# Performance work log

Measured on AMD Instinct MI355X. Metric: run time of the kernel, lower is better.

Reference implementation:

```python
import jax, jax.numpy as jnp
import numpy as np

S, L, E, H, HID, T = 4096, 16, 256, 512, 512, 50
CHAR_V = 128


def _lstm_scan(x, W_ih, W_hh, b):
    """x: [T, B, D] -> all hidden states [T, B, H]. PyTorch gate order i,f,g,o.
    b is the sum of torch's b_ih + b_hh (identical math)."""
    Hh = W_hh.shape[1]
    B = x.shape[1]

    def cell(carry, xt):
        h, c = carry
        g = xt @ W_ih.T + h @ W_hh.T + b  # [B, 4H]
        i, f, gg, o = jnp.split(g, 4, axis=-1)
        c = jax.nn.sigmoid(f) * c + jax.nn.sigmoid(i) * jnp.tanh(gg)
        h = jax.nn.sigmoid(o) * jnp.tanh(c)
        return (h, c), h

    init = (jnp.zeros((B, Hh), x.dtype), jnp.zeros((B, Hh), x.dtype))
    _, hs = jax.lax.scan(cell, init, x)
    return hs


def setup_inputs() -> dict:
    key = jax.random.key(0)
    ks = jax.random.split(key, 18)

    def p(k, shape):
        return jax.random.normal(k, shape, jnp.float32) * 0.05

    return {
        "chars": jax.random.randint(ks[0], (S, L), 0, CHAR_V),
        "char_lens": jax.random.randint(ks[1], (S,), 0, L),
        "char_table": p(ks[2], (CHAR_V, E)),
        "cW_ih": p(ks[3], (4 * E, E)),
        "cW_hh": p(ks[4], (4 * E, E)),
        "cb": p(ks[5], (4 * E,)),
        "W_ih0": p(ks[6], (2, 4 * H, E)),
        "W_hh0": p(ks[7], (2, 4 * H, H)),
        "b0": p(ks[8], (2, 4 * H)),
        "W_ih1": p(ks[9], (2, 4 * H, 2 * H)),
        "W_hh1": p(ks[10], (2, 4 * H, H)),
        "b1": p(ks[11], (2, 4 * H)),
        "fc1_w": p(ks[12], (HID, 2 * H)),
        "fc1_b": p(ks[13], (HID,)),
        "fc2_w": p(ks[14], (T, HID)),
        "fc2_b": p(ks[15], (T,)),
    }


def reference(chars, char_lens, char_table, cW_ih, cW_hh, cb,
              W_ih0, W_hh0, b0, W_ih1, W_hh1, b1,
              fc1_w, fc1_b, fc2_w, fc2_b):
    n_words = chars.shape[0]
    # --- char LSTM: batched over all words (replaces per-word python loop) ---
    emb = char_table[chars]                               # [S, L, E]
    hs = _lstm_scan(emb.transpose(1, 0, 2), cW_ih, cW_hh, cb)  # [L, S, E]
    lens = jnp.maximum(char_lens, 1)                      # every word has >=1 char
    word_emb = hs[lens - 1, jnp.arange(n_words)]          # hn per word: [S, E]

    # --- 2-layer bidirectional sentence LSTM, batch = 1 ---
    x = word_emb[:, None, :]                              # [S, 1, E]

    def bi_layer(x, Wih, Whh, b):
        fwd = _lstm_scan(x, Wih[0], Whh[0], b[0])
        bwd = _lstm_scan(x[::-1], Wih[1], Whh[1], b[1])[::-1]
        return jnp.concatenate([fwd, bwd], axis=-1)       # [S, 1, 2H]

    x = bi_layer(x, W_ih0, W_hh0, b0)
    x = bi_layer(x, W_ih1, W_hh1, b1)

    # --- MLP head ---
    out = x[:, 0, :]                                      # [S, 2H]
    out = jnp.tanh(out @ fc1_w.T + fc1_b)                 # [S, HID]
    return out @ fc2_w.T + fc2_b                          # [S, T]
```

## Files before the change

### kernel.cpp

```cpp
#include <hip/hip_runtime.h>
#include <math.h>
#include <stdint.h>


#define NPOS 4096
#define GDIM 2048

typedef short short8 __attribute__((ext_vector_type(8)));
typedef float f32x4 __attribute__((ext_vector_type(4)));

__device__ __forceinline__ float sigf(float x) { return 1.0f / (1.0f + __expf(-x)); }
__device__ __forceinline__ float tanh_fast(float x) {
  float e = __expf(2.f * x);
  return 1.f - 2.f / (e + 1.f);
}
__device__ __forceinline__ unsigned int pack_bf16(float a, float b) {
  unsigned int ua = __float_as_uint(a), ub = __float_as_uint(b);
  ua = (ua + 0x7fffu + ((ua >> 16) & 1u)) >> 16;
  ub = (ub + 0x7fffu + ((ub >> 16) & 1u)) >> 16;
  return ua | (ub << 16);
}
__device__ __forceinline__ unsigned short bf16_1(float a) {
  unsigned int ua = __float_as_uint(a);
  return (unsigned short)((ua + 0x7fffu + ((ua >> 16) & 1u)) >> 16);
}
__device__ __forceinline__ float bf2f(unsigned short s) {
  return __uint_as_float(((unsigned int)s) << 16);
}

__global__ __launch_bounds__(256) void build_wc_kernel(
    const float* __restrict__ cWih, const float* __restrict__ cWhh,
    unsigned int* __restrict__ Wc)
{
  const int idx = blockIdx.x * 256 + threadIdx.x;
  const int g = idx >> 8;
  const int k = (idx & 255) * 2;
  const float* src = (k < 256) ? (cWih + (size_t)g * 256 + k)
                               : (cWhh + (size_t)g * 256 + (k - 256));
  Wc[idx] = pack_bf16(src[0], src[1]);
}

__global__ __launch_bounds__(256) void mfchar_kernel(
    const int* __restrict__ chars, const int* __restrict__ lens,
    const float* __restrict__ table, const unsigned short* __restrict__ Wc,
    const float* __restrict__ cb, float* __restrict__ word_emb)
{
  __shared__ unsigned short uL[32][520];
  __shared__ unsigned short gL[32][1032];
  __shared__ int sidx[32];
  const int tid = threadIdx.x;
  const int lane = tid & 63;
  const int wv = tid >> 6;
  const int w0 = blockIdx.x * 32;
  if (tid < 32) { int l = lens[w0 + tid]; sidx[tid] = (l < 1 ? 1 : l) - 1; }
  for (int i = tid; i < 32 * 256; i += 256) uL[i >> 8][256 + (i & 255)] = 0;

  float bz[16];
  #pragma unroll
  for (int ni = 0; ni < 16; ++ni) bz[ni] = cb[wv * 256 + ni * 16 + (lane & 15)];

  float c[32];
  #pragma unroll
  for (int w = 0; w < 32; ++w) c[w] = 0.f;

  const int arow = lane & 15;
  const int akk = (lane >> 4) * 8;

  for (int t = 0; t < 16; ++t) {
    for (int w = 0; w < 32; ++w) {
      const int cid = chars[(w0 + w) * 16 + t];
      uL[w][tid] = bf16_1(table[(size_t)cid * 256 + tid]);
    }
    __syncthreads();

    f32x4 acc[2][16];
    #pragma unroll
    for (int mi = 0; mi < 2; ++mi)
      #pragma unroll
      for (int ni = 0; ni < 16; ++ni)
        acc[mi][ni] = (f32x4){bz[ni], bz[ni], bz[ni], bz[ni]};
    for (int kt = 0; kt < 16; ++kt) {
      short8 af0 = *(const short8*)&uL[arow][kt * 32 + akk];
      short8 af1 = *(const short8*)&uL[16 + arow][kt * 32 + akk];
      #pragma unroll
      for (int ni = 0; ni < 16; ++ni) {
        const unsigned short* bp =
            Wc + (size_t)(wv * 256 + ni * 16 + arow) * 512 + kt * 32 + akk;
        short8 bf = *(const short8*)bp;
        acc[0][ni] = __builtin_amdgcn_mfma_f32_16x16x32_bf16(af0, bf, acc[0][ni], 0, 0, 0);
        acc[1][ni] = __builtin_amdgcn_mfma_f32_16x16x32_bf16(af1, bf, acc[1][ni], 0, 0, 0);
      }
    }
    #pragma unroll
    for (int mi = 0; mi < 2; ++mi)
      #pragma unroll
      for (int ni = 0; ni < 16; ++ni) {
        const int col = wv * 256 + ni * 16 + (lane & 15);
        #pragma unroll
        for (int r = 0; r < 4; ++r) {
          const int row = mi * 16 + (lane >> 4) * 4 + r;
          gL[row][col] = bf16_1(acc[mi][ni][r]);
        }
      }
    __syncthreads();

    const int j = tid;
    #pragma unroll 4
    for (int w = 0; w < 32; ++w) {
      const float iv = sigf(bf2f(gL[w][j]));
      const float fv = sigf(bf2f(gL[w][256 + j]));
      const float gv = tanh_fast(bf2f(gL[w][512 + j]));
      const float ov = sigf(bf2f(gL[w][768 + j]));
      c[w] = fv * c[w] + iv * gv;
      const float h = ov * tanh_fast(c[w]);
      uL[w][256 + j] = bf16_1(h);
      if (t == sidx[w]) word_emb[(size_t)(w0 + w) * 256 + j] = h;
    }
    __syncthreads();
  }
}

#define SW(c) ((c) + (((c) >> 3) << 2))
template <int SPLIT, int ACT, int PERM>
__global__ __launch_bounds__(256) void gemm_kernel(
    const float* __restrict__ A, const float* __restrict__ A2,
    const float* __restrict__ B, const float* __restrict__ bias,
    float* __restrict__ C, int M, int N, int K)
{
  __shared__ float At[8 * 192];
  __shared__ float Bt[8 * 192];
  const int tid = threadIdx.x;
  const int bm0 = blockIdx.x * 128, bn0 = blockIdx.y * 128;
  float acc[8][8];
  #pragma unroll
  for (int i = 0; i < 8; ++i)
    #pragma unroll
    for (int j = 0; j < 8; ++j) acc[i][j] = 0.f;
  const int sr = tid >> 1;
  const int sk = (tid & 1) * 4;
  const int tm = (tid >> 4) * 8, tn = (tid & 15) * 8;
  const int swsr = SW(sr);
  const int stm = SW(tm), stn = SW(tn);
  for (int k0 = 0; k0 < K; k0 += 8) {
    const int kg = k0 + sk;
    float4 av;
    if (SPLIT) {
      const float* srcp = (kg < 512) ? A : A2;
      av = *(const float4*)(srcp + (size_t)(bm0 + sr) * 512 + (kg & 511));
    } else {
      av = *(const float4*)(A + (size_t)(bm0 + sr) * K + kg);
    }
    float4 bv = {0.f, 0.f, 0.f, 0.f};
    if (bn0 + sr < N) bv = *(const float4*)(B + (size_t)(bn0 + sr) * K + kg);
    At[(sk + 0) * 192 + swsr] = av.x; At[(sk + 1) * 192 + swsr] = av.y;
    At[(sk + 2) * 192 + swsr] = av.z; At[(sk + 3) * 192 + swsr] = av.w;
    Bt[(sk + 0) * 192 + swsr] = bv.x; Bt[(sk + 1) * 192 + swsr] = bv.y;
    Bt[(sk + 2) * 192 + swsr] = bv.z; Bt[(sk + 3) * 192 + swsr] = bv.w;
    __syncthreads();
    #pragma unroll
    for (int kk = 0; kk < 8; ++kk) {
      float a[8], b[8];
      *(float4*)&a[0] = *(const float4*)&At[kk * 192 + stm];
      *(float4*)&a[4] = *(const float4*)&At[kk * 192 + stm + 4];
      *(float4*)&b[0] = *(const float4*)&Bt[kk * 192 + stn];
      *(float4*)&b[4] = *(const float4*)&Bt[kk * 192 + stn + 4];
      #pragma unroll
      for (int i = 0; i < 8; ++i)
        #pragma unroll
        for (int j = 0; j < 8; ++j) acc[i][j] = fmaf(a[i], b[j], acc[i][j]);
    }
    __syncthreads();
  }
  #pragma unroll
  for (int i = 0; i < 8; ++i) {
    const int m = bm0 + tm + i;
    float* crow = C + (size_t)m * N;
    #pragma unroll
    for (int j = 0; j < 8; ++j) {
      const int n = bn0 + tn + j;
      if (n < N) {
        float v = acc[i][j] + bias[n];
        if (ACT) v = tanhf(v);
        if (PERM) crow[((n & 511) << 2) | (n >> 9)] = v;
        else      crow[n] = v;
      }
    }
  }
}

template <int SPLIT, int ACT, int PERM>
__global__ __launch_bounds__(256) void mfgemm_kernel(
    const float* __restrict__ A, const float* __restrict__ A2,
    const float* __restrict__ B, const float* __restrict__ bias,
    float* __restrict__ C, int M, int N, int K)
{
  __shared__ unsigned short AL[128 * 40];
  __shared__ unsigned short BL[128 * 40];
  const int tid = threadIdx.x;
  const int bm0 = blockIdx.x * 128, bn0 = blockIdx.y * 128;
  const int srow = tid >> 1;
  const int sk = (tid & 1) * 16;
  const int lane = tid & 63;
  const int wid = tid >> 6;
  const int wm0 = (wid >> 1) * 64;
  const int wn0 = (wid & 1) * 64;
  const int lrow = lane & 15;
  const int lk = (lane >> 4) * 8;

  f32x4 acc[4][4];
  #pragma unroll
  for (int i = 0; i < 4; ++i)
    #pragma unroll
    for (int j = 0; j < 4; ++j) acc[i][j] = (f32x4){0.f, 0.f, 0.f, 0.f};

  for (int k0 = 0; k0 < K; k0 += 32) {
    const int kg = k0 + sk;
    float av[16], bv[16];
    if (SPLIT) {
      const float* srcp = (kg < 512) ? A : A2;
      const float* ap = srcp + (size_t)(bm0 + srow) * 512 + (kg & 511);
      #pragma unroll
      for (int i = 0; i < 4; ++i) *(float4*)&av[4 * i] = ((const float4*)ap)[i];
    } else {
      const float* ap = A + (size_t)(bm0 + srow) * K + kg;
      #pragma unroll
      for (int i = 0; i < 4; ++i) *(float4*)&av[4 * i] = ((const float4*)ap)[i];
    }
    {
      const float* bp = B + (size_t)(bn0 + srow) * K + kg;
      #pragma unroll
      for (int i = 0; i < 4; ++i) *(float4*)&bv[4 * i] = ((const float4*)bp)[i];
    }
    unsigned int pa[8], pb[8];
    #pragma unroll
    for (int i = 0; i < 8; ++i) {
      pa[i] = pack_bf16(av[2 * i], av[2 * i + 1]);
      pb[i] = pack_bf16(bv[2 * i], bv[2 * i + 1]);
    }
    unsigned short* adst = &AL[srow * 40 + sk];
    unsigned short* bdst = &BL[srow * 40 + sk];
    *(uint4*)adst       = *(uint4*)&pa[0];
    *(uint4*)(adst + 8) = *(uint4*)&pa[4];
    *(uint4*)bdst       = *(uint4*)&pb[0];
    *(uint4*)(bdst + 8) = *(uint4*)&pb[4];
    __syncthreads();

    short8 af[4], bf[4];
    #pragma unroll
    for (int mi = 0; mi < 4; ++mi)
      af[mi] = *(const short8*)&AL[(wm0 + mi * 16 + lrow) * 40 + lk];
    #pragma unroll
    for (int ni = 0; ni < 4; ++ni)
      bf[ni] = *(const short8*)&BL[(wn0 + ni * 16 + lrow) * 40 + lk];
    #pragma unroll
    for (int mi = 0; mi < 4; ++mi)
      #pragma unroll
      for (int ni = 0; ni < 4; ++ni)
        acc[mi][ni] = __builtin_amdgcn_mfma_f32_16x16x32_bf16(
            af[mi], bf[ni], acc[mi][ni], 0, 0, 0);
    __syncthreads();
  }

  #pragma unroll
  for (int mi = 0; mi < 4; ++mi) {
    #pragma unroll
    for (int ni = 0; ni < 4; ++ni) {
      const int n = bn0 + wn0 + ni * 16 + (lane & 15);
      const float bz = bias[n];
      const int nw = PERM ? (((n & 511) << 2) | (n >> 9)) : n;
      #pragma unroll
      for (int r = 0; r < 4; ++r) {
        const int m = bm0 + wm0 + mi * 16 + (lane >> 4) * 4 + r;
        float v = acc[mi][ni][r] + bz;
        if (ACT) v = tanhf(v);
        C[(size_t)m * N + nw] = v;
      }
    }
  }
}

__global__ __launch_bounds__(512) void scan_kernel(
    const float* __restrict__ Xf, const float* __restrict__ Xb,
    const float* __restrict__ Whf, const float* __restrict__ Whb,
    unsigned long long* __restrict__ Tf, unsigned long long* __restrict__ Tb,
    float* __restrict__ Hf, float* __restrict__ Hb)
{
  __shared__ float lds_h[2][576];
  const int tid = threadIdx.x;
  const int dir = blockIdx.x & 1;
  const int wg  = blockIdx.x >> 1;
  const float* X = dir ? Xb : Xf;
  const float* Wh = dir ? Whb : Whf;
  unsigned long long* T = dir ? Tb : Tf;
  float* Hd = dir ? Hb : Hf;

  const int row8 = tid >> 3;
  const int klane = tid & 7;
  const int u = row8 >> 2, g = row8 & 3;
  const int R = g * 512 + wg * 16 + u;

  float wreg[64];
  {
    const float* wrow = Wh + (size_t)R * 512 + klane * 64;
    #pragma unroll
    for (int i = 0; i < 16; ++i) {
      float4 v = ((const float4*)wrow)[i];
      wreg[4 * i] = v.x; wreg[4 * i + 1] = v.y; wreg[4 * i + 2] = v.z; wreg[4 * i + 3] = v.w;
    }
  }
  const int l0 = 72 * klane;
  const int l1 = l0 + 36;
  const int la = tid + ((tid >> 5) << 2);
  const int rep = wg & 3;

  for (int i = tid; i < 576; i += 512) lds_h[0][i] = 0.f;

  const bool xl = (klane == 0);
  const int xoff = wg * 64 + row8;
  float xcur = 0.f, xnxt = 0.f;
  if (xl) {
    xcur = X[(size_t)(dir ? NPOS - 1 : 0) * GDIM + xoff];
    xnxt = X[(size_t)(dir ? NPOS - 2 : 1) * GDIM + xoff];
  }
  float creg = 0.f;
  __syncthreads();

  for (int s = 0; s < NPOS; ++s) {
    const int p = dir ? (NPOS - 1 - s) : s;
    if (s > 0) {
      const unsigned int tg = (unsigned int)s;
      const unsigned long long* w =
          T + (size_t)((rep << 1) | ((s - 1) & 1)) * 512 + tid;
      unsigned long long v;
      do { v = __hip_atomic_load(w, __ATOMIC_RELAXED, __HIP_MEMORY_SCOPE_AGENT); }
      while ((unsigned int)(v >> 32) != tg);
      lds_h[s & 1][la] = __uint_as_float((unsigned int)v);
    }
    __syncthreads();
    const float* hb = &lds_h[s & 1][0];
    float sA = xl ? xcur : 0.f, sB = 0.f, sC = 0.f, sD = 0.f;
    if (xl) {
      xcur = xnxt;
      if (s + 2 < NPOS) xnxt = X[(size_t)(dir ? NPOS - 3 - s : s + 2) * GDIM + xoff];
    }
    #pragma unroll
    for (int i = 0; i < 4; ++i) {
      float4 a = *(const float4*)&hb[l0 + 4 * i];
      sA = fmaf(wreg[4 * i + 0], a.x, sA);
      sA = fmaf(wreg[4 * i + 1], a.y, sA);
      sA = fmaf(wreg[4 * i + 2], a.z, sA);
      sA = fmaf(wreg[4 * i + 3], a.w, sA);
      float4 b = *(const float4*)&hb[l0 + 16 + 4 * i];
      sB = fmaf(wreg[16 + 4 * i + 0], b.x, sB);
      sB = fmaf(wreg[16 + 4 * i + 1], b.y, sB);
      sB = fmaf(wreg[16 + 4 * i + 2], b.z, sB);
      sB = fmaf(wreg[16 + 4 * i + 3], b.w, sB);
      float4 c = *(const float4*)&hb[l1 + 4 * i];
      sC = fmaf(wreg[32 + 4 * i + 0], c.x, sC);
      sC = fmaf(wreg[32 + 4 * i + 1], c.y, sC);
      sC = fmaf(wreg[32 + 4 * i + 2], c.z, sC);
      sC = fmaf(wreg[32 + 4 * i + 3], c.w, sC);
      float4 d = *(const float4*)&hb[l1 + 16 + 4 * i];
      sD = fmaf(wreg[48 + 4 * i + 0], d.x, sD);
      sD = fmaf(wreg[48 + 4 * i + 1], d.y, sD);
      sD = fmaf(wreg[48 + 4 * i + 2], d.z, sD);
      sD = fmaf(wreg[48 + 4 * i + 3], d.w, sD);
    }
    float sum = (sA + sB) + (sC + sD);
    sum += __shfl_xor(sum, 1);
    sum += __shfl_xor(sum, 2);
    sum += __shfl_xor(sum, 4);
    const int base = (tid & 63) & ~31;
    float gf = __shfl(sum, base + 8);
    float gg = __shfl(sum, base + 16);
    float go = __shfl(sum, base + 24);
    if ((tid & 31) == 0) {
      float iv = sigf(sum), fv = sigf(gf), gv = tanh_fast(gg), ov = sigf(go);
      creg = fv * creg + iv * gv;
      float h = ov * tanh_fast(creg);
      const int j = wg * 16 + u;
      unsigned long long pack = ((unsigned long long)(unsigned int)(s + 1) << 32)
                              | (unsigned long long)__float_as_uint(h);
      #pragma unroll
      for (int r2 = 0; r2 < 4; ++r2)
        __hip_atomic_store(&T[(size_t)((r2 << 1) | (s & 1)) * 512 + j], pack,
                           __ATOMIC_RELAXED, __HIP_MEMORY_SCOPE_AGENT);
      Hd[(size_t)p * 512 + j] = h;
    }
  }
}

extern "C" void kernel_launch(void* const* d_in, const int* in_sizes, int n_in,
                              void* d_out, int out_size, void* d_ws, size_t ws_size,
                              hipStream_t stream) {
  const int* chars = (const int*)d_in[0];
  const int* lens = (const int*)d_in[1];
  const float* table = (const float*)d_in[2];
  const float* cWih = (const float*)d_in[3];
  const float* cWhh = (const float*)d_in[4];
  const float* cb = (const float*)d_in[5];
  const float* Wih0 = (const float*)d_in[6];
  const float* Whh0 = (const float*)d_in[7];
  const float* b0 = (const float*)d_in[8];
  const float* Wih1 = (const float*)d_in[9];
  const float* Whh1 = (const float*)d_in[10];
  const float* b1 = (const float*)d_in[11];
  const float* fc1w = (const float*)d_in[12];
  const float* fc1b = (const float*)d_in[13];
  const float* fc2w = (const float*)d_in[14];
  const float* fc2b = (const float*)d_in[15];
  float* out = (float*)d_out;

  char* ws = (char*)d_ws;
  size_t off = 0;
  auto alloc = [&](size_t bytes) -> void* {
    void* p = ws + off;
    off += (bytes + 255) & ~(size_t)255;
    return p;
  };
  float* word_emb = (float*)alloc((size_t)4096 * 256 * 4);
  float* X0f = (float*)alloc((size_t)4096 * 2048 * 4);
  float* X0b = (float*)alloc((size_t)4096 * 2048 * 4);
  float* H0f = (float*)alloc((size_t)4096 * 512 * 4);
  float* H0b = (float*)alloc((size_t)4096 * 512 * 4);
  float* H1f = (float*)alloc((size_t)4096 * 512 * 4);
  float* H1b = (float*)alloc((size_t)4096 * 512 * 4);
  float* fc1out = (float*)alloc((size_t)4096 * 512 * 4);
  unsigned int* Wc = (unsigned int*)alloc((size_t)1024 * 512 * 2);
  unsigned long long* Tall = (unsigned long long*)alloc((size_t)4 * 4096 * 8);
  unsigned long long* T0f = Tall;
  unsigned long long* T0b = Tall + 4096;
  unsigned long long* T1f = Tall + 8192;
  unsigned long long* T1b = Tall + 12288;
  if (off > ws_size) return;

  hipMemsetAsync(Tall, 0, (size_t)4 * 4096 * 8, stream);

  build_wc_kernel<<<1024, 256, 0, stream>>>(cWih, cWhh, Wc);
  mfchar_kernel<<<128, 256, 0, stream>>>(chars, lens, table,
                                         (const unsigned short*)Wc, cb, word_emb);

  mfgemm_kernel<0, 0, 1><<<dim3(32, 16), 256, 0, stream>>>(
      word_emb, nullptr, Wih0, b0, X0f, 4096, 2048, 256);
  mfgemm_kernel<0, 0, 1><<<dim3(32, 16), 256, 0, stream>>>(
      word_emb, nullptr, Wih0 + (size_t)2048 * 256, b0 + 2048, X0b, 4096, 2048, 256);
  scan_kernel<<<64, 512, 0, stream>>>(X0f, X0b, Whh0, Whh0 + (size_t)2048 * 512,
                                      T0f, T0b, H0f, H0b);

  mfgemm_kernel<1, 0, 1><<<dim3(32, 16), 256, 0, stream>>>(
      H0f, H0b, Wih1, b1, X0f, 4096, 2048, 1024);
  mfgemm_kernel<1, 0, 1><<<dim3(32, 16), 256, 0, stream>>>(
      H0f, H0b, Wih1 + (size_t)2048 * 1024, b1 + 2048, X0b, 4096, 2048, 1024);
  scan_kernel<<<64, 512, 0, stream>>>(X0f, X0b, Whh1, Whh1 + (size_t)2048 * 512,
                                      T1f, T1b, H1f, H1b);

  mfgemm_kernel<1, 1, 0><<<dim3(32, 4), 256, 0, stream>>>(
      H1f, H1b, fc1w, fc1b, fc1out, 4096, 512, 1024);
  gemm_kernel<0, 0, 0><<<dim3(32, 1), 256, 0, stream>>>(
      fc1out, nullptr, fc2w, fc2b, out, 4096, 50, 512);
}
```

Before: 13.94 ms.

## Fuse LSTM input projection into the recurrent scan kernel

Removes the separate input-projection GEMMs and their large X buffers. Each scan workgroup now keeps its slice of W_ih in registers as packed bf16 and computes x·W_ih + b per timestep. The input row is staged into double-buffered LDS, and the product is computed before the cross-block spin-wait so it can overlap that latency. The cost is extra per-step FMAs and LDS reads on the serial path, plus heavy register pressure (64 fp32 W_hh plus up to 64 packed W_ih values per thread at 512 threads), which risks spills.

New measurement: 37.03 ms. 2.66x slower.

```diff
diff --git a/kernel.cpp b/kernel.cpp
--- a/kernel.cpp
+++ b/kernel.cpp
@@ -4,7 +4,6 @@
 
 
 #define NPOS 4096
-#define GDIM 2048
 
 typedef short short8 __attribute__((ext_vector_type(8)));
 typedef float f32x4 __attribute__((ext_vector_type(4)));
@@ -121,7 +120,7 @@
 }
 
 #define SW(c) ((c) + (((c) >> 3) << 2))
-template <int SPLIT, int ACT, int PERM>
+template <int SPLIT, int ACT>
 __global__ __launch_bounds__(256) void gemm_kernel(
     const float* __restrict__ A, const float* __restrict__ A2,
     const float* __restrict__ B, const float* __restrict__ bias,
@@ -181,14 +180,13 @@
       if (n < N) {
         float v = acc[i][j] + bias[n];
         if (ACT) v = tanhf(v);
-        if (PERM) crow[((n & 511) << 2) | (n >> 9)] = v;
-        else      crow[n] = v;
+        crow[n] = v;
       }
     }
   }
 }
 
-template <int SPLIT, int ACT, int PERM>
+template <int SPLIT, int ACT>
 __global__ __launch_bounds__(256) void mfgemm_kernel(
     const float* __restrict__ A, const float* __restrict__ A2,
     const float* __restrict__ B, const float* __restrict__ bias,
@@ -267,30 +265,36 @@
     for (int ni = 0; ni < 4; ++ni) {
       const int n = bn0 + wn0 + ni * 16 + (lane & 15);
       const float bz = bias[n];
-      const int nw = PERM ? (((n & 511) << 2) | (n >> 9)) : n;
       #pragma unroll
       for (int r = 0; r < 4; ++r) {
         const int m = bm0 + wm0 + mi * 16 + (lane >> 4) * 4 + r;
         float v = acc[mi][ni][r] + bz;
         if (ACT) v = tanhf(v);
-        C[(size_t)m * N + nw] = v;
+        C[(size_t)m * N + n] = v;
       }
     }
   }
 }
 
-__global__ __launch_bounds__(512) void scan_kernel(
-    const float* __restrict__ Xf, const float* __restrict__ Xb,
-    const float* __restrict__ Whf, const float* __restrict__ Whb,
+template <int K_IN, int SPLIT>
+__global__ __launch_bounds__(512) void scan_fused_kernel(
+    const float* __restrict__ U1, const float* __restrict__ U2,
+    const float* __restrict__ Wih,
+    const float* __restrict__ bias,
+    const float* __restrict__ Whh,
     unsigned long long* __restrict__ Tf, unsigned long long* __restrict__ Tb,
     float* __restrict__ Hf, float* __restrict__ Hb)
 {
+  constexpr int KS = K_IN / 8;
+  constexpr int UP = KS + 4;
   __shared__ float lds_h[2][576];
+  __shared__ float uL[2][8 * UP];
   const int tid = threadIdx.x;
   const int dir = blockIdx.x & 1;
   const int wg  = blockIdx.x >> 1;
-  const float* X = dir ? Xb : Xf;
-  const float* Wh = dir ? Whb : Whf;
+  const float* Wh = Whh + (size_t)dir * 2048 * 512;
+  const float* Wx = Wih + (size_t)dir * 2048 * K_IN;
+  const float* bs = bias + (size_t)dir * 2048;
   unsigned long long* T = dir ? Tb : Tf;
   float* Hd = dir ? Hb : Hf;
 
@@ -308,25 +312,59 @@
       wreg[4 * i] = v.x; wreg[4 * i + 1] = v.y; wreg[4 * i + 2] = v.z; wreg[4 * i + 3] = v.w;
     }
   }
+  unsigned int wih[KS / 2];
+  {
+    const float* wr = Wx + (size_t)R * K_IN + klane * KS;
+    #pragma unroll
+    for (int j = 0; j < KS / 2; ++j) wih[j] = pack_bf16(wr[2 * j], wr[2 * j + 1]);
+  }
+  const float bz = (klane == 0) ? bs[R] : 0.f;
+
   const int l0 = 72 * klane;
   const int l1 = l0 + 36;
   const int la = tid + ((tid >> 5) << 2);
   const int rep = wg & 3;
 
+  auto loadU = [&](int p) -> float2 {
+    float2 r = {0.f, 0.f};
+    if (SPLIT) {
+      if (tid < 256) r = *(const float2*)&U1[(size_t)p * 512 + 2 * tid];
+      else           r = *(const float2*)&U2[(size_t)p * 512 + 2 * (tid - 256)];
+    } else if (tid < K_IN / 2) {
+      r = *(const float2*)&U1[(size_t)p * K_IN + 2 * tid];
+    }
+    return r;
+  };
+  auto storeU = [&](float2 v, int buf) {
+    if (SPLIT || tid < K_IN / 2) {
+      const int k = 2 * tid;
+      const int pos = k + (k / KS) * 4;
+      uL[buf][pos] = v.x;
+      uL[buf][pos + 1] = v.y;
+    }
+  };
+
   for (int i = tid; i < 576; i += 512) lds_h[0][i] = 0.f;
-
-  const bool xl = (klane == 0);
-  const int xoff = wg * 64 + row8;
-  float xcur = 0.f, xnxt = 0.f;
-  if (xl) {
-    xcur = X[(size_t)(dir ? NPOS - 1 : 0) * GDIM + xoff];
-    xnxt = X[(size_t)(dir ? NPOS - 2 : 1) * GDIM + xoff];
-  }
+  { float2 v0 = loadU(dir ? NPOS - 1 : 0); storeU(v0, 0); }
+  float2 regU = loadU(dir ? NPOS - 2 : 1);
   float creg = 0.f;
   __syncthreads();
 
   for (int s = 0; s < NPOS; ++s) {
     const int p = dir ? (NPOS - 1 - s) : s;
+
+    const float* ub = &uL[s & 1][klane * UP];
+    float xp = bz, xq = 0.f;
+    #pragma unroll
+    for (int j = 0; j < KS / 4; ++j) {
+      float4 a = *(const float4*)&ub[4 * j];
+      const unsigned int w0 = wih[2 * j], w1 = wih[2 * j + 1];
+      xp = fmaf(__uint_as_float(w0 << 16), a.x, xp);
+      xq = fmaf(__uint_as_float(w0 & 0xffff0000u), a.y, xq);
+      xp = fmaf(__uint_as_float(w1 << 16), a.z, xp);
+      xq = fmaf(__uint_as_float(w1 & 0xffff0000u), a.w, xq);
+    }
+
     if (s > 0) {
       const unsigned int tg = (unsigned int)s;
       const unsigned long long* w =
@@ -336,13 +374,11 @@
       while ((unsigned int)(v >> 32) != tg);
       lds_h[s & 1][la] = __uint_as_float((unsigned int)v);
     }
-    __syncthreads();
+    if (s + 1 < NPOS) storeU(regU, (s + 1) & 1);
+    __syncthreads();
+
     const float* hb = &lds_h[s & 1][0];
-    float sA = xl ? xcur : 0.f, sB = 0.f, sC = 0.f, sD = 0.f;
-    if (xl) {
-      xcur = xnxt;
-      if (s + 2 < NPOS) xnxt = X[(size_t)(dir ? NPOS - 3 - s : s + 2) * GDIM + xoff];
-    }
+    float sA = xp, sB = xq, sC = 0.f, sD = 0.f;
     #pragma unroll
     for (int i = 0; i < 4; ++i) {
       float4 a = *(const float4*)&hb[l0 + 4 * i];
@@ -387,6 +423,7 @@
                            __ATOMIC_RELAXED, __HIP_MEMORY_SCOPE_AGENT);
       Hd[(size_t)p * 512 + j] = h;
     }
+    if (s + 2 < NPOS) regU = loadU(dir ? NPOS - 3 - s : s + 2);
   }
 }
 
@@ -419,8 +456,6 @@
     return p;
   };
   float* word_emb = (float*)alloc((size_t)4096 * 256 * 4);
-  float* X0f = (float*)alloc((size_t)4096 * 2048 * 4);
-  float* X0b = (float*)alloc((size_t)4096 * 2048 * 4);
   float* H0f = (float*)alloc((size_t)4096 * 512 * 4);
   float* H0b = (float*)alloc((size_t)4096 * 512 * 4);
   float* H1f = (float*)alloc((size_t)4096 * 512 * 4);
@@ -440,22 +475,13 @@
   mfchar_kernel<<<128, 256, 0, stream>>>(chars, lens, table,
                                          (const unsigned short*)Wc, cb, word_emb);
 
-  mfgemm_kernel<0, 0, 1><<<dim3(32, 16), 256, 0, stream>>>(
-      word_emb, nullptr, Wih0, b0, X0f, 4096, 2048, 256);
-  mfgemm_kernel<0, 0, 1><<<dim3(32, 16), 256, 0, stream>>>(
-      word_emb, nullptr, Wih0 + (size_t)2048 * 256, b0 + 2048, X0b, 4096, 2048, 256);
-  scan_kernel<<<64, 512, 0, stream>>>(X0f, X0b, Whh0, Whh0 + (size_t)2048 * 512,
-                                      T0f, T0b, H0f, H0b);
-
-  mfgemm_kernel<1, 0, 1><<<dim3(32, 16), 256, 0, stream>>>(
-      H0f, H0b, Wih1, b1, X0f, 4096, 2048, 1024);
-  mfgemm_kernel<1, 0, 1><<<dim3(32, 16), 256, 0, stream>>>(
-      H0f, H0b, Wih1 + (size_t)2048 * 1024, b1 + 2048, X0b, 4096, 2048, 1024);
-  scan_kernel<<<64, 512, 0, stream>>>(X0f, X0b, Whh1, Whh1 + (size_t)2048 * 512,
-                                      T1f, T1b, H1f, H1b);
-
-  mfgemm_kernel<1, 1, 0><<<dim3(32, 4), 256, 0, stream>>>(
+  scan_fused_kernel<256, 0><<<64, 512, 0, stream>>>(
+      word_emb, nullptr, Wih0, b0, Whh0, T0f, T0b, H0f, H0b);
+  scan_fused_kernel<1024, 1><<<64, 512, 0, stream>>>(
+      H0f, H0b, Wih1, b1, Whh1, T1f, T1b, H1f, H1b);
+
+  mfgemm_kernel<1, 1><<<dim3(32, 4), 256, 0, stream>>>(
       H1f, H1b, fc1w, fc1b, fc1out, 4096, 512, 1024);
-  gemm_kernel<0, 0, 0><<<dim3(32, 1), 256, 0, stream>>>(
+  gemm_kernel<0, 0><<<dim3(32, 1), 256, 0, stream>>>(
       fc1out, nullptr, fc2w, fc2b, out, 4096, 50, 512);
 }
```
